# Kernel optimization log

Hardware: AMD Instinct MI355X
Metric: run time of the kernel (lower is better)

## Reference

```python
import jax, jax.numpy as jnp
import numpy as np

# NeuralVolume(num_levels=4, level_dim=8, base_resolution=16, per_level_scale=2)
RESOLUTIONS = [16, 32, 64, 128]          # ceil(16 * 2**l) per level
LEVEL_DIM = 8                             # C
OFFSETS = np.concatenate([[0], np.cumsum([r ** 3 for r in RESOLUTIONS])]).astype(np.int64)
N_PARAMS = int(OFFSETS[-1])               # 2,396,160 (dense grids, no hashing: R^3 << 2^24)
B = 1 << 20
# 8 cube corners, d=0 is the fastest-varying (stride-1) dim as in the CUDA kernel
CORNERS = np.array([[i, j, k] for k in (0, 1) for j in (0, 1) for i in (0, 1)], np.int32)


def setup_inputs() -> dict:
    key = jax.random.key(0)
    k1, k2 = jax.random.split(key)
    inputs = jax.random.uniform(k1, (B, 3), dtype=jnp.float32)          # coords in [0,1)
    embeddings = jax.random.normal(k2, (N_PARAMS, LEVEL_DIM), dtype=jnp.float32) * 1e-4
    return {"inputs": inputs, "embeddings": embeddings}


def _encode_level(x, table, R):
    # x: [B,3] in [0,1]; table: [R^3, C] dense grid for this level
    scale = jnp.float32(R - 1)
    pos = x * scale                                   # [B,3]
    pg = jnp.floor(pos)
    frac = pos - pg                                   # [B,3] trilinear fractions
    pg = pg.astype(jnp.int32)
    corners = jnp.asarray(CORNERS)                    # [8,3]
    cg = jnp.clip(pg[:, None, :] + corners[None], 0, R - 1)   # [B,8,3]
    # linear index with stride 1 along d=0 (index += pos_grid[d]*stride; stride *= R)
    idx = cg[..., 0] + cg[..., 1] * R + cg[..., 2] * (R * R)  # [B,8]
    w = jnp.prod(jnp.where(corners[None] == 1, frac[:, None, :], 1.0 - frac[:, None, :]), axis=-1)  # [B,8]
    feats = table[idx]                                # [B,8,C] irregular gather
    return jnp.einsum('bk,bkc->bc', w, feats)         # [B,C]


def reference(inputs, embeddings):
    outs = []
    for l, R in enumerate(RESOLUTIONS):
        table = jax.lax.dynamic_slice_in_dim(embeddings, int(OFFSETS[l]), int(OFFSETS[l + 1] - OFFSETS[l]), axis=0)
        outs.append(_encode_level(inputs, table, R))
    return jnp.concatenate(outs, axis=-1)             # [B, L*C] = [B, 32]
```

## Files before the change

### kernel.cpp

```cpp
#include <hip/hip_runtime.h>

#define LEVEL_DIM 8
#define CDIM 32
#define NCELLS (CDIM*CDIM*CDIM)
#define NGROUPS (NCELLS/8)

#define SLAB_ROWS 1307

typedef float    f32x4 __attribute__((ext_vector_type(4)));
typedef unsigned u32x4 __attribute__((ext_vector_type(4)));

__device__ __forceinline__ unsigned part1by2(unsigned x) {
    x &= 0x3ff;
    x = (x | (x << 16)) & 0x030000FF;
    x = (x | (x << 8))  & 0x0300F00F;
    x = (x | (x << 4))  & 0x030C30C3;
    x = (x | (x << 2))  & 0x09249249;
    return x;
}
__device__ __forceinline__ unsigned compact1by2(unsigned x) {
    x &= 0x09249249;
    x = (x | (x >> 2))  & 0x030C30C3;
    x = (x | (x >> 4))  & 0x0300F00F;
    x = (x | (x >> 8))  & 0x030000FF;
    x = (x | (x >> 16)) & 0x000003FF;
    return x;
}

__device__ __forceinline__ int cell_of(float x, float y, float z) {
    int cx = min(CDIM - 1, max(0, (int)(x * (float)CDIM)));
    int cy = min(CDIM - 1, max(0, (int)(y * (float)CDIM)));
    int cz = min(CDIM - 1, max(0, (int)(z * (float)CDIM)));
    return (int)(part1by2(cx) | (part1by2(cy) << 1) | (part1by2(cz) << 2));
}

__device__ __forceinline__ unsigned pk_bf16(float a, float b) {
    unsigned ua = __float_as_uint(a), ub = __float_as_uint(b);
    ua += 0x7fffu + ((ua >> 16) & 1u);
    ub += 0x7fffu + ((ub >> 16) & 1u);
    return (ua >> 16) | (ub & 0xffff0000u);
}

__global__ __launch_bounds__(256) void nv_hist(
    const float* __restrict__ in, int* __restrict__ hist,
    unsigned* __restrict__ cellrank, int B)
{
    const int b = blockIdx.x * 256 + threadIdx.x;
    if (b >= B) return;
    const float x = in[3 * b], y = in[3 * b + 1], z = in[3 * b + 2];
    const int c = cell_of(x, y, z);
    const unsigned r = (unsigned)atomicAdd(&hist[c], 1);
    cellrank[b] = (unsigned)c | (r << 15);
}

__global__ __launch_bounds__(1024) void nv_scan(int* __restrict__ cell)
{
    __shared__ int lds[1024];
    const int tid = threadIdx.x;
    const int base = tid * (NCELLS / 1024);
    int v[NCELLS / 1024];
    int s = 0;
    #pragma unroll
    for (int e = 0; e < NCELLS / 1024; ++e) { v[e] = cell[base + e]; s += v[e]; }
    lds[tid] = s;
    __syncthreads();
    for (int off = 1; off < 1024; off <<= 1) {
        int t = 0;
        if (tid >= off) t = lds[tid - off];
        __syncthreads();
        if (tid >= off) lds[tid] += t;
        __syncthreads();
    }
    int run = lds[tid] - s;
    #pragma unroll
    for (int e = 0; e < NCELLS / 1024; ++e) { cell[base + e] = run; run += v[e]; }
}

__global__ __launch_bounds__(256) void nv_scatter(
    const float* __restrict__ in, const int* __restrict__ starts,
    const unsigned* __restrict__ cellrank, f32x4* __restrict__ sorted, int B)
{
    const int b = blockIdx.x * 256 + threadIdx.x;
    if (b >= B) return;
    const float x = in[3 * b], y = in[3 * b + 1], z = in[3 * b + 2];
    const unsigned cr = cellrank[b];
    const int pos = starts[cr & 0x7fffu] + (int)(cr >> 15);
    f32x4 v = { x, y, z, __uint_as_float((unsigned)b) };
    sorted[pos] = v;
}


template<int R, int S, int BASE, int TOFF>
__device__ __forceinline__ void stage_level(
    const float* __restrict__ emb, unsigned* slab,
    int s0x, int s0y, int s0z, int tid)
{
    const float* tbl = emb + (size_t)TOFF * LEVEL_DIM;
    constexpr int ROWS = S * S * S;
    #pragma unroll
    for (int t0 = 0; t0 < ROWS; t0 += 256) {
        const int t = t0 + tid;
        if (t < ROWS) {
            const int lx = t % S;
            const int tm = t / S;
            const int ly = tm % S;
            const int lz = tm / S;
            const float* src = tbl +
                ((size_t)((s0z + lz) * R + (s0y + ly)) * R + (s0x + lx)) * LEVEL_DIM;
            const f32x4 a = *(const f32x4*)src;
            const f32x4 b = *(const f32x4*)(src + 4);
            u32x4 d = { pk_bf16(a.x, a.y), pk_bf16(a.z, a.w),
                        pk_bf16(b.x, b.y), pk_bf16(b.z, b.w) };
            *(u32x4*)&slab[(BASE + t) * 4] = d;
        }
    }
}

__device__ __forceinline__ void fma_row(float w, u32x4 d, float* acc) {
    acc[0] = fmaf(w, __uint_as_float(d.x << 16),         acc[0]);
    acc[1] = fmaf(w, __uint_as_float(d.x & 0xffff0000u), acc[1]);
    acc[2] = fmaf(w, __uint_as_float(d.y << 16),         acc[2]);
    acc[3] = fmaf(w, __uint_as_float(d.y & 0xffff0000u), acc[3]);
    acc[4] = fmaf(w, __uint_as_float(d.z << 16),         acc[4]);
    acc[5] = fmaf(w, __uint_as_float(d.z & 0xffff0000u), acc[5]);
    acc[6] = fmaf(w, __uint_as_float(d.w << 16),         acc[6]);
    acc[7] = fmaf(w, __uint_as_float(d.w & 0xffff0000u), acc[7]);
}

template<int R, int S, int BASE>
__device__ __forceinline__ void enc_level(
    const unsigned* slab, int s0x, int s0y, int s0z,
    float x, float y, float z, float* accp)
{
    const float scale = (float)(R - 1);
    const float px = x * scale, py = y * scale, pz = z * scale;
    const float gx = floorf(px), gy = floorf(py), gz = floorf(pz);
    const float fx = px - gx, fy = py - gy, fz = pz - gz;
    const int ix = (int)gx, iy = (int)gy, iz = (int)gz;

    const int ix0 = min(max(ix, 0), R - 1);
    const int ix1 = min(max(ix + 1, 0), R - 1);
    const int iy0 = min(max(iy, 0), R - 1);
    const int iy1 = min(max(iy + 1, 0), R - 1);
    const int iz0 = min(max(iz, 0), R - 1);
    const int iz1 = min(max(iz + 1, 0), R - 1);

    const int lx0 = ix0 - s0x, lx1 = ix1 - s0x;
    const int ly0 = iy0 - s0y, ly1 = iy1 - s0y;
    const int lz0 = iz0 - s0z, lz1 = iz1 - s0z;

    const float wx0 = 1.0f - fx, wx1 = fx;

    float acc[8];
    #pragma unroll
    for (int c = 0; c < 8; ++c) acc[c] = 0.0f;

    #pragma unroll
    for (int kk = 0; kk < 2; ++kk) {
        const int   lz = kk ? lz1 : lz0;
        const float wz = kk ? fz : (1.0f - fz);
        #pragma unroll
        for (int jj = 0; jj < 2; ++jj) {
            const int   ly = jj ? ly1 : ly0;
            const float wy = jj ? fy : (1.0f - fy);

            const int rb = BASE + (lz * S + ly) * S;
            const u32x4 d0 = *(const u32x4*)&slab[(rb + lx0) * 4];
            const u32x4 d1 = *(const u32x4*)&slab[(rb + lx1) * 4];

            fma_row((wx0 * wy) * wz, d0, acc);
            fma_row((wx1 * wy) * wz, d1, acc);
        }
    }
    #pragma unroll
    for (int c = 0; c < 8; ++c) accp[c] = acc[c];
}

__global__ __launch_bounds__(256) void nv_encode_group(
    const f32x4* __restrict__ sorted,
    const int* __restrict__ starts,
    const float* __restrict__ emb,
    float* __restrict__ out,
    int B)
{
    __shared__ __align__(16) unsigned slab[SLAB_ROWS * 4];
    __shared__ __align__(16) float obuf[4][32 * 36];

    int grp = (int)blockIdx.x;
    grp = (grp & 7) * (NGROUPS / 8) + (grp >> 3);

    const int c0 = grp << 3;
    const int start = starts[c0];
    const int end   = (c0 + 8 < NCELLS) ? starts[c0 + 8] : B;
    if (start >= end) return;

    const int gx = (int)compact1by2((unsigned)grp);
    const int gy = (int)compact1by2((unsigned)grp >> 1);
    const int gz = (int)compact1by2((unsigned)grp >> 2);

    const int s0x0 = min((gx * 30)  >> 5, 13),  s0y0 = min((gy * 30)  >> 5, 13),  s0z0 = min((gz * 30)  >> 5, 13);
    const int s0x1 = min((gx * 62)  >> 5, 28),  s0y1 = min((gy * 62)  >> 5, 28),  s0z1 = min((gz * 62)  >> 5, 28);
    const int s0x2 = min((gx * 126) >> 5, 58),  s0y2 = min((gy * 126) >> 5, 58),  s0z2 = min((gz * 126) >> 5, 58);
    const int s0x3 = min((gx * 254) >> 5, 118), s0y3 = min((gy * 254) >> 5, 118), s0z3 = min((gz * 254) >> 5, 118);

    const int tid = threadIdx.x;
    stage_level<16,  3,  0,   0>     (emb, slab, s0x0, s0y0, s0z0, tid);
    stage_level<32,  4,  27,  4096>  (emb, slab, s0x1, s0y1, s0z1, tid);
    stage_level<64,  6,  91,  36864> (emb, slab, s0x2, s0y2, s0z2, tid);
    stage_level<128, 10, 307, 299008>(emb, slab, s0x3, s0y3, s0z3, tid);
    __syncthreads();

    const int wave = tid >> 6;
    const int lane = tid & 63;
    float* wbuf = &obuf[wave][0];

    for (int p0 = start + wave * 64; p0 < end; p0 += 256) {
        const int p = p0 + lane;
        const bool valid = p < end;

        float acc[32];
        unsigned ob = 0;
        if (valid) {
            const f32x4 s = sorted[p];
            ob = __float_as_uint(s.w);
            enc_level<16,  3,  0>  (slab, s0x0, s0y0, s0z0, s.x, s.y, s.z, &acc[0]);
            enc_level<32,  4,  27> (slab, s0x1, s0y1, s0z1, s.x, s.y, s.z, &acc[8]);
            enc_level<64,  6,  91> (slab, s0x2, s0y2, s0z2, s.x, s.y, s.z, &acc[16]);
            enc_level<128, 10, 307>(slab, s0x3, s0y3, s0z3, s.x, s.y, s.z, &acc[24]);
        }

        #pragma unroll
        for (int h = 0; h < 2; ++h) {
            asm volatile("s_waitcnt lgkmcnt(0)" ::: "memory");
            if (valid && (lane >> 5) == h) {
                const int q = lane & 31;
                #pragma unroll
                for (int k = 0; k < 8; ++k)
                    *(f32x4*)&wbuf[q * 36 + k * 4] = *(const f32x4*)&acc[k * 4];
            }
            asm volatile("s_waitcnt lgkmcnt(0)" ::: "memory");
            #pragma unroll
            for (int j = 0; j < 4; ++j) {
                const int slot = j * 8 + (lane >> 3);
                const int i = h * 32 + slot;
                const unsigned obi = __shfl(ob, i);
                if (p0 + i < end) {
                    const f32x4 v = *(const f32x4*)
                        &wbuf[slot * 36 + (lane & 7) * 4];
                    __builtin_nontemporal_store(
                        v, (f32x4*)(out + (size_t)obi * 32 + (lane & 7) * 4));
                }
            }
        }
    }
}

__global__ __launch_bounds__(256) void nv_encode_direct(
    const float* __restrict__ in,
    const float* __restrict__ emb,
    float* __restrict__ out,
    int B)
{
    const int i = blockIdx.x * 256 + threadIdx.x;
    if (i >= B) return;
    const float x = in[3 * i], y = in[3 * i + 1], z = in[3 * i + 2];
    float* op = out + (size_t)i * 32;

    const int RES[4] = {16, 32, 64, 128};
    const int OFF[4] = {0, 4096, 36864, 299008};

    #pragma unroll
    for (int l = 0; l < 4; ++l) {
        const int R = RES[l];
        const float scale = (float)(R - 1);
        const float px = x * scale, py = y * scale, pz = z * scale;
        const float gxf = floorf(px), gyf = floorf(py), gzf = floorf(pz);
        const float fx = px - gxf, fy = py - gyf, fz = pz - gzf;
        const int ix = (int)gxf, iy = (int)gyf, iz = (int)gzf;
        const int ix0 = min(max(ix, 0), R - 1), ix1 = min(max(ix + 1, 0), R - 1);
        const int iy0 = min(max(iy, 0), R - 1), iy1 = min(max(iy + 1, 0), R - 1);
        const int iz0 = min(max(iz, 0), R - 1), iz1 = min(max(iz + 1, 0), R - 1);
        const float* tbl = emb + (size_t)OFF[l] * LEVEL_DIM;
        const float wx0 = 1.0f - fx, wx1 = fx;
        float acc[8];
        #pragma unroll
        for (int c = 0; c < 8; ++c) acc[c] = 0.0f;
        #pragma unroll
        for (int kk = 0; kk < 2; ++kk) {
            const int zz = kk ? iz1 : iz0;
            const float wz = kk ? fz : (1.0f - fz);
            #pragma unroll
            for (int jj = 0; jj < 2; ++jj) {
                const int yy = jj ? iy1 : iy0;
                const float wy = jj ? fy : (1.0f - fy);
                const size_t rowbase = ((size_t)zz * R + yy) * (size_t)R;
                const float* r0 = tbl + (rowbase + ix0) * LEVEL_DIM;
                const float* r1 = tbl + (rowbase + ix1) * LEVEL_DIM;
                const float w0 = (wx0 * wy) * wz;
                const float w1 = (wx1 * wy) * wz;
                const float4 a0 = *(const float4*)(r0);
                const float4 a1 = *(const float4*)(r0 + 4);
                const float4 b0 = *(const float4*)(r1);
                const float4 b1 = *(const float4*)(r1 + 4);
                acc[0] = fmaf(w0, a0.x, acc[0]); acc[1] = fmaf(w0, a0.y, acc[1]);
                acc[2] = fmaf(w0, a0.z, acc[2]); acc[3] = fmaf(w0, a0.w, acc[3]);
                acc[4] = fmaf(w0, a1.x, acc[4]); acc[5] = fmaf(w0, a1.y, acc[5]);
                acc[6] = fmaf(w0, a1.z, acc[6]); acc[7] = fmaf(w0, a1.w, acc[7]);
                acc[0] = fmaf(w1, b0.x, acc[0]); acc[1] = fmaf(w1, b0.y, acc[1]);
                acc[2] = fmaf(w1, b0.z, acc[2]); acc[3] = fmaf(w1, b0.w, acc[3]);
                acc[4] = fmaf(w1, b1.x, acc[4]); acc[5] = fmaf(w1, b1.y, acc[5]);
                acc[6] = fmaf(w1, b1.z, acc[6]); acc[7] = fmaf(w1, b1.w, acc[7]);
            }
        }
        *(float4*)(op + l * 8)     = make_float4(acc[0], acc[1], acc[2], acc[3]);
        *(float4*)(op + l * 8 + 4) = make_float4(acc[4], acc[5], acc[6], acc[7]);
    }
}

extern "C" void kernel_launch(void* const* d_in, const int* in_sizes, int n_in,
                              void* d_out, int out_size, void* d_ws, size_t ws_size,
                              hipStream_t stream) {
    const float* in  = (const float*)d_in[0];
    const float* emb = (const float*)d_in[1];
    float* out = (float*)d_out;

    const int B = in_sizes[0] / 3;
    const int block = 256;
    const int grid = (B + block - 1) / block;

    const size_t hist_bytes = (size_t)NCELLS * sizeof(int);
    const size_t rank_bytes = (size_t)B * sizeof(unsigned);
    const size_t need = hist_bytes + rank_bytes + (size_t)B * sizeof(f32x4);

    if (ws_size >= need) {
        int*      hist     = (int*)d_ws;
        unsigned* cellrank = (unsigned*)((char*)d_ws + hist_bytes);
        f32x4*    sorted   = (f32x4*)((char*)d_ws + hist_bytes + rank_bytes);

        (void)hipMemsetAsync(hist, 0, hist_bytes, stream);
        nv_hist<<<grid, block, 0, stream>>>(in, hist, cellrank, B);
        nv_scan<<<1, 1024, 0, stream>>>(hist);
        nv_scatter<<<grid, block, 0, stream>>>(in, hist, cellrank, sorted, B);
        nv_encode_group<<<NGROUPS, 256, 0, stream>>>(sorted, hist, emb, out, B);
    } else {
        nv_encode_direct<<<grid, block, 0, stream>>>(in, emb, out, B);
    }
}
```

Before: 126.6 us.

## Split each point across 8 lanes by level and channel half, drop LDS transpose

```diff
diff --git a/kernel.cpp b/kernel.cpp
--- a/kernel.cpp
+++ b/kernel.cpp
@@ -116,66 +116,6 @@
     }
 }
 
-__device__ __forceinline__ void fma_row(float w, u32x4 d, float* acc) {
-    acc[0] = fmaf(w, __uint_as_float(d.x << 16),         acc[0]);
-    acc[1] = fmaf(w, __uint_as_float(d.x & 0xffff0000u), acc[1]);
-    acc[2] = fmaf(w, __uint_as_float(d.y << 16),         acc[2]);
-    acc[3] = fmaf(w, __uint_as_float(d.y & 0xffff0000u), acc[3]);
-    acc[4] = fmaf(w, __uint_as_float(d.z << 16),         acc[4]);
-    acc[5] = fmaf(w, __uint_as_float(d.z & 0xffff0000u), acc[5]);
-    acc[6] = fmaf(w, __uint_as_float(d.w << 16),         acc[6]);
-    acc[7] = fmaf(w, __uint_as_float(d.w & 0xffff0000u), acc[7]);
-}
-
-template<int R, int S, int BASE>
-__device__ __forceinline__ void enc_level(
-    const unsigned* slab, int s0x, int s0y, int s0z,
-    float x, float y, float z, float* accp)
-{
-    const float scale = (float)(R - 1);
-    const float px = x * scale, py = y * scale, pz = z * scale;
-    const float gx = floorf(px), gy = floorf(py), gz = floorf(pz);
-    const float fx = px - gx, fy = py - gy, fz = pz - gz;
-    const int ix = (int)gx, iy = (int)gy, iz = (int)gz;
-
-    const int ix0 = min(max(ix, 0), R - 1);
-    const int ix1 = min(max(ix + 1, 0), R - 1);
-    const int iy0 = min(max(iy, 0), R - 1);
-    const int iy1 = min(max(iy + 1, 0), R - 1);
-    const int iz0 = min(max(iz, 0), R - 1);
-    const int iz1 = min(max(iz + 1, 0), R - 1);
-
-    const int lx0 = ix0 - s0x, lx1 = ix1 - s0x;
-    const int ly0 = iy0 - s0y, ly1 = iy1 - s0y;
-    const int lz0 = iz0 - s0z, lz1 = iz1 - s0z;
-
-    const float wx0 = 1.0f - fx, wx1 = fx;
-
-    float acc[8];
-    #pragma unroll
-    for (int c = 0; c < 8; ++c) acc[c] = 0.0f;
-
-    #pragma unroll
-    for (int kk = 0; kk < 2; ++kk) {
-        const int   lz = kk ? lz1 : lz0;
-        const float wz = kk ? fz : (1.0f - fz);
-        #pragma unroll
-        for (int jj = 0; jj < 2; ++jj) {
-            const int   ly = jj ? ly1 : ly0;
-            const float wy = jj ? fy : (1.0f - fy);
-
-            const int rb = BASE + (lz * S + ly) * S;
-            const u32x4 d0 = *(const u32x4*)&slab[(rb + lx0) * 4];
-            const u32x4 d1 = *(const u32x4*)&slab[(rb + lx1) * 4];
-
-            fma_row((wx0 * wy) * wz, d0, acc);
-            fma_row((wx1 * wy) * wz, d1, acc);
-        }
-    }
-    #pragma unroll
-    for (int c = 0; c < 8; ++c) accp[c] = acc[c];
-}
-
 __global__ __launch_bounds__(256) void nv_encode_group(
     const f32x4* __restrict__ sorted,
     const int* __restrict__ starts,
@@ -184,7 +124,6 @@
     int B)
 {
     __shared__ __align__(16) unsigned slab[SLAB_ROWS * 4];
-    __shared__ __align__(16) float obuf[4][32 * 36];
 
     int grp = (int)blockIdx.x;
     grp = (grp & 7) * (NGROUPS / 8) + (grp >> 3);
@@ -210,48 +149,72 @@
     stage_level<128, 10, 307, 299008>(emb, slab, s0x3, s0y3, s0z3, tid);
     __syncthreads();
 
-    const int wave = tid >> 6;
-    const int lane = tid & 63;
-    float* wbuf = &obuf[wave][0];
-
-    for (int p0 = start + wave * 64; p0 < end; p0 += 256) {
-        const int p = p0 + lane;
-        const bool valid = p < end;
-
-        float acc[32];
-        unsigned ob = 0;
-        if (valid) {
-            const f32x4 s = sorted[p];
-            ob = __float_as_uint(s.w);
-            enc_level<16,  3,  0>  (slab, s0x0, s0y0, s0z0, s.x, s.y, s.z, &acc[0]);
-            enc_level<32,  4,  27> (slab, s0x1, s0y1, s0z1, s.x, s.y, s.z, &acc[8]);
-            enc_level<64,  6,  91> (slab, s0x2, s0y2, s0z2, s.x, s.y, s.z, &acc[16]);
-            enc_level<128, 10, 307>(slab, s0x3, s0y3, s0z3, s.x, s.y, s.z, &acc[24]);
-        }
-
-        #pragma unroll
-        for (int h = 0; h < 2; ++h) {
-            asm volatile("s_waitcnt lgkmcnt(0)" ::: "memory");
-            if (valid && (lane >> 5) == h) {
-                const int q = lane & 31;
-                #pragma unroll
-                for (int k = 0; k < 8; ++k)
-                    *(f32x4*)&wbuf[q * 36 + k * 4] = *(const f32x4*)&acc[k * 4];
-            }
-            asm volatile("s_waitcnt lgkmcnt(0)" ::: "memory");
-            #pragma unroll
-            for (int j = 0; j < 4; ++j) {
-                const int slot = j * 8 + (lane >> 3);
-                const int i = h * 32 + slot;
-                const unsigned obi = __shfl(ob, i);
-                if (p0 + i < end) {
-                    const f32x4 v = *(const f32x4*)
-                        &wbuf[slot * 36 + (lane & 7) * 4];
-                    __builtin_nontemporal_store(
-                        v, (f32x4*)(out + (size_t)obi * 32 + (lane & 7) * 4));
-                }
-            }
-        }
+    const int ln  = tid & 7;
+    const int lvl = ln >> 1;
+    const int sub = tid >> 3;
+
+    #define SEL4(v0,v1,v2,v3) ((lvl & 2) ? ((lvl & 1) ? (v3) : (v2)) \
+                                         : ((lvl & 1) ? (v1) : (v0)))
+    const float scale = SEL4(15.0f, 31.0f, 63.0f, 127.0f);
+    const int   Rm1   = SEL4(15, 31, 63, 127);
+    const int   S_    = SEL4(3, 4, 6, 10);
+    const int   BASE_ = SEL4(0, 27, 91, 307);
+    const int   sx    = SEL4(s0x0, s0x1, s0x2, s0x3);
+    const int   sy    = SEL4(s0y0, s0y1, s0y2, s0y3);
+    const int   sz    = SEL4(s0z0, s0z1, s0z2, s0z3);
+    #undef SEL4
+    const int dsel = (ln & 1) * 2;
+
+    for (int p = start + sub; p < end; p += 32) {
+        const f32x4 s = sorted[p];
+        const unsigned ob = __float_as_uint(s.w);
+
+        const float px = s.x * scale, py = s.y * scale, pz = s.z * scale;
+        const float gpx = floorf(px), gpy = floorf(py), gpz = floorf(pz);
+        const float fx = px - gpx, fy = py - gpy, fz = pz - gpz;
+        const int ix = (int)gpx, iy = (int)gpy, iz = (int)gpz;
+
+        const int ix0 = min(max(ix, 0), Rm1),     ix1 = min(max(ix + 1, 0), Rm1);
+        const int iy0 = min(max(iy, 0), Rm1),     iy1 = min(max(iy + 1, 0), Rm1);
+        const int iz0 = min(max(iz, 0), Rm1),     iz1 = min(max(iz + 1, 0), Rm1);
+
+        const int lx0 = ix0 - sx, lx1 = ix1 - sx;
+        const int ly0 = iy0 - sy, ly1 = iy1 - sy;
+        const int lz0 = iz0 - sz, lz1 = iz1 - sz;
+
+        const float wx0 = 1.0f - fx, wx1 = fx;
+        const float wy0 = 1.0f - fy, wy1 = fy;
+        const float wz0 = 1.0f - fz, wz1 = fz;
+
+        const int rzy00 = BASE_ + (lz0 * S_ + ly0) * S_;
+        const int rzy01 = BASE_ + (lz0 * S_ + ly1) * S_;
+        const int rzy10 = BASE_ + (lz1 * S_ + ly0) * S_;
+        const int rzy11 = BASE_ + (lz1 * S_ + ly1) * S_;
+
+        float a0 = 0.0f, a1 = 0.0f, a2 = 0.0f, a3 = 0.0f;
+
+        #define CORNER(rzy, lx, wx, wy, wz) do {                              \
+            const uint2 d = *(const uint2*)&slab[((rzy) + (lx)) * 4 + dsel];  \
+            const float w = ((wx) * (wy)) * (wz);                             \
+            a0 = fmaf(w, __uint_as_float(d.x << 16),         a0);             \
+            a1 = fmaf(w, __uint_as_float(d.x & 0xffff0000u), a1);             \
+            a2 = fmaf(w, __uint_as_float(d.y << 16),         a2);             \
+            a3 = fmaf(w, __uint_as_float(d.y & 0xffff0000u), a3);             \
+        } while (0)
+
+        CORNER(rzy00, lx0, wx0, wy0, wz0);
+        CORNER(rzy00, lx1, wx1, wy0, wz0);
+        CORNER(rzy01, lx0, wx0, wy1, wz0);
+        CORNER(rzy01, lx1, wx1, wy1, wz0);
+        CORNER(rzy10, lx0, wx0, wy0, wz1);
+        CORNER(rzy10, lx1, wx1, wy0, wz1);
+        CORNER(rzy11, lx0, wx0, wy1, wz1);
+        CORNER(rzy11, lx1, wx1, wy1, wz1);
+        #undef CORNER
+
+        const f32x4 r = { a0, a1, a2, a3 };
+        __builtin_nontemporal_store(
+            r, (f32x4*)(out + (size_t)ob * 32 + ln * 4));
     }
 }
 
```

New measurement: 122.0 us. -3.6%, faster.
